# Kernel tuning notes

Hardware: AMD Instinct MI355X
Metric: run time of the kernel (lower is better)

## Reference

```python
import jax, jax.numpy as jnp
import numpy as np
import math

HIDDEN = 2048
N_Q = 16
N_KV = 8
HEAD_DIM = 128
THETA = 10000.0
RANK = 8
ALPHA = 16
LORA_SCALING = ALPHA / RANK  # 2.0
SCALING = 1.0 / math.sqrt(HEAD_DIM)


def setup_inputs() -> dict:
    key = jax.random.key(0)
    ks = jax.random.split(key, 14)
    B, S = 2, 2048
    std = 0.02
    inp = {
        "x": jax.random.normal(ks[0], (B, S, HIDDEN), dtype=jnp.float32),
        # nn.Linear weights: [out_features, in_features]
        "Wq": jax.random.normal(ks[1], (N_Q * HEAD_DIM, HIDDEN), dtype=jnp.float32) * std,
        "Wk": jax.random.normal(ks[2], (N_KV * HEAD_DIM, HIDDEN), dtype=jnp.float32) * std,
        "Wv": jax.random.normal(ks[3], (N_KV * HEAD_DIM, HIDDEN), dtype=jnp.float32) * std,
        "Wo": jax.random.normal(ks[4], (HIDDEN, N_Q * HEAD_DIM), dtype=jnp.float32) * std,
        "qA": jax.random.normal(ks[5], (RANK, HIDDEN), dtype=jnp.float32) * std,
        "qB": jax.random.normal(ks[6], (N_Q * HEAD_DIM, RANK), dtype=jnp.float32) * std,
        "kA": jax.random.normal(ks[7], (RANK, HIDDEN), dtype=jnp.float32) * std,
        "kB": jax.random.normal(ks[8], (N_KV * HEAD_DIM, RANK), dtype=jnp.float32) * std,
        "vA": jax.random.normal(ks[9], (RANK, HIDDEN), dtype=jnp.float32) * std,
        "vB": jax.random.normal(ks[10], (N_KV * HEAD_DIM, RANK), dtype=jnp.float32) * std,
        "oA": jax.random.normal(ks[11], (RANK, N_Q * HEAD_DIM), dtype=jnp.float32) * std,
        "oB": jax.random.normal(ks[12], (HIDDEN, RANK), dtype=jnp.float32) * std,
    }
    return inp


def _rope_cos_sin(seq_len, dtype):
    inv_freq = 1.0 / (THETA ** (jnp.arange(0, HEAD_DIM, 2, dtype=jnp.float32) / HEAD_DIM))
    t = jnp.arange(seq_len, dtype=jnp.float32)
    freqs = t[:, None] * inv_freq[None, :]  # [S, D/2]
    return jnp.cos(freqs).astype(dtype), jnp.sin(freqs).astype(dtype)


def _apply_rope(x, cos, sin):
    # x: [B, H, S, D]; interleaved real/imag pairs on last dim
    xr = x[..., ::2]
    xi = x[..., 1::2]
    rr = xr * cos - xi * sin
    ri = xr * sin + xi * cos
    return jnp.stack([rr, ri], axis=-1).reshape(x.shape)


def _forward(x, Wq, Wk, Wv, Wo, qA, qB, kA, kB, vA, vB, oA, oB):
    B, S, H = x.shape
    # base projections + LoRA (low-rank path kept factored: (x @ A^T) @ B^T)
    q = x @ Wq.T + ((x @ qA.T) @ qB.T) * LORA_SCALING  # [B,S,NQ*D]
    k = x @ Wk.T + ((x @ kA.T) @ kB.T) * LORA_SCALING  # [B,S,NKV*D]
    v = x @ Wv.T + ((x @ vA.T) @ vB.T) * LORA_SCALING
    q = q.reshape(B, S, N_Q, HEAD_DIM).transpose(0, 2, 1, 3)   # [B,NQ,S,D]
    k = k.reshape(B, S, N_KV, HEAD_DIM).transpose(0, 2, 1, 3)  # [B,NKV,S,D]
    v = v.reshape(B, S, N_KV, HEAD_DIM).transpose(0, 2, 1, 3)
    cos, sin = _rope_cos_sin(S, x.dtype)  # [S, D/2] each
    q = _apply_rope(q, cos, sin)
    k = _apply_rope(k, cos, sin)
    if N_Q != N_KV:
        rep = N_Q // N_KV
        k = jnp.repeat(k, rep, axis=1)  # [B,NQ,S,D]
        v = jnp.repeat(v, rep, axis=1)
    scores = jnp.einsum('bhqd,bhkd->bhqk', q, k) * SCALING
    causal = jnp.tril(jnp.ones((S, S), dtype=bool))
    scores = jnp.where(causal, scores, -jnp.inf)
    attn = jax.nn.softmax(scores, axis=-1).astype(v.dtype)
    out = jnp.einsum('bhqk,bhkd->bhqd', attn, v)  # [B,NQ,S,D]
    out = out.transpose(0, 2, 1, 3).reshape(B, S, N_Q * HEAD_DIM)
    return out @ Wo.T + ((out @ oA.T) @ oB.T) * LORA_SCALING


def reference(x, Wq, Wk, Wv, Wo, qA, qB, kA, kB, vA, vB, oA, oB):
    return _forward(x, Wq, Wk, Wv, Wo, qA, qB, kA, kB, vA, vB, oA, oB)
```

## Files before the change

### kernel.cpp

```cpp
#include <hip/hip_runtime.h>
#include <hip/hip_bf16.h>
#include <cmath>

#define HIDDEN 2048
#define SEQ 2048
#define BATCH 2
#define NQ 16
#define NKV 8
#define HD 128
#define RANKL 8
#define LORA_SCALE 2.0f
#define INV_SQRT_D 0.08838834764831845f
#define LOG2E 1.4426950408889634f
#define SM_SCALE (INV_SQRT_D * LOG2E)

typedef unsigned short ushort_t;
typedef __bf16 bf16x8 __attribute__((ext_vector_type(8)));
typedef float f32x4 __attribute__((ext_vector_type(4)));

static __device__ __forceinline__ ushort_t f2bf(float f) {
    __hip_bfloat16 h = __float2bfloat16(f);
    return *(ushort_t*)&h;
}
static __device__ __forceinline__ float bf2f(ushort_t u) {
    unsigned int v = ((unsigned int)u) << 16;
    return __builtin_bit_cast(float, v);
}
static __device__ __forceinline__ void gload_lds16(const ushort_t* g, ushort_t* l) {
    __builtin_amdgcn_global_load_lds(
        (const __attribute__((address_space(1))) unsigned int*)g,
        (__attribute__((address_space(3))) unsigned int*)l, 16, 0, 0);
}

__global__ __launch_bounds__(256) void lora_cast_x(
    const float* __restrict__ X, ushort_t* __restrict__ Xbf,
    const float* __restrict__ qA, const float* __restrict__ kA,
    const float* __restrict__ vA,
    float* __restrict__ oq, float* __restrict__ ok, float* __restrict__ ov)
{
    int m = blockIdx.x;
    int t = threadIdx.x;
    int c0 = t * 8;
    const float* xr = X + (size_t)m * HIDDEN + c0;
    float4 a = *(const float4*)xr;
    float4 b = *(const float4*)(xr + 4);
    float xv[8] = {a.x, a.y, a.z, a.w, b.x, b.y, b.z, b.w};
    uint4 o;
    o.x = (unsigned int)f2bf(xv[0]) | ((unsigned int)f2bf(xv[1]) << 16);
    o.y = (unsigned int)f2bf(xv[2]) | ((unsigned int)f2bf(xv[3]) << 16);
    o.z = (unsigned int)f2bf(xv[4]) | ((unsigned int)f2bf(xv[5]) << 16);
    o.w = (unsigned int)f2bf(xv[6]) | ((unsigned int)f2bf(xv[7]) << 16);
    *(uint4*)(Xbf + (size_t)m * HIDDEN + c0) = o;

    float p[3][RANKL];
#pragma unroll
    for (int w = 0; w < 3; w++)
#pragma unroll
        for (int r = 0; r < RANKL; r++) p[w][r] = 0.f;
    const float* Aw[3] = {qA, kA, vA};
#pragma unroll
    for (int e = 0; e < 8; e++) {
        float x8 = xv[e];
#pragma unroll
        for (int w = 0; w < 3; w++)
#pragma unroll
            for (int r = 0; r < RANKL; r++)
                p[w][r] += x8 * Aw[w][r * HIDDEN + c0 + e];
    }
#pragma unroll
    for (int w = 0; w < 3; w++)
#pragma unroll
        for (int r = 0; r < RANKL; r++) {
            float v = p[w][r];
            v += __shfl_xor(v, 32); v += __shfl_xor(v, 16);
            v += __shfl_xor(v, 8);  v += __shfl_xor(v, 4);
            v += __shfl_xor(v, 2);  v += __shfl_xor(v, 1);
            p[w][r] = v;
        }
    __shared__ float wred[4][3][RANKL];
    int wave = t >> 6, lane = t & 63;
    if (lane == 0) {
#pragma unroll
        for (int w = 0; w < 3; w++)
#pragma unroll
            for (int r = 0; r < RANKL; r++) wred[wave][w][r] = p[w][r];
    }
    __syncthreads();
    if (t < 3 * RANKL) {
        int w = t / RANKL, r = t % RANKL;
        float s = wred[0][w][r] + wred[1][w][r] + wred[2][w][r] + wred[3][w][r];
        float* dst = (w == 0) ? oq : (w == 1) ? ok : ov;
        dst[(size_t)m * RANKL + r] = s;
    }
}

__global__ __launch_bounds__(256) void lora_xa_bf16(
    const ushort_t* __restrict__ X, const float* __restrict__ Aw,
    float* __restrict__ out, int K)
{
    int m = blockIdx.x;
    int t = threadIdx.x;
    const ushort_t* xr = X + (size_t)m * K;
    float p[RANKL];
#pragma unroll
    for (int r = 0; r < RANKL; r++) p[r] = 0.f;
    for (int c = t; c < K; c += 256) {
        float xv = bf2f(xr[c]);
#pragma unroll
        for (int r = 0; r < RANKL; r++) p[r] += xv * Aw[r * K + c];
    }
#pragma unroll
    for (int r = 0; r < RANKL; r++) {
        float v = p[r];
        v += __shfl_xor(v, 32); v += __shfl_xor(v, 16);
        v += __shfl_xor(v, 8);  v += __shfl_xor(v, 4);
        v += __shfl_xor(v, 2);  v += __shfl_xor(v, 1);
        p[r] = v;
    }
    __shared__ float wred[4][RANKL];
    int wave = t >> 6, lane = t & 63;
    if (lane == 0) {
#pragma unroll
        for (int r = 0; r < RANKL; r++) wred[wave][r] = p[r];
    }
    __syncthreads();
    if (t < RANKL) {
        out[(size_t)m * RANKL + t] =
            wred[0][t] + wred[1][t] + wred[2][t] + wred[3][t];
    }
}

__global__ __launch_bounds__(256) void cast_weights(
    const float* __restrict__ Wq, const float* __restrict__ Wk,
    const float* __restrict__ Wv, const float* __restrict__ Wo,
    ushort_t* __restrict__ Wqb, ushort_t* __restrict__ Wkb,
    ushort_t* __restrict__ Wvb, ushort_t* __restrict__ Wob)
{
    size_t i = (size_t)blockIdx.x * 256 + threadIdx.x;
    const float* src; ushort_t* dst; size_t j;
    if (i < 524288)       { src = Wq; dst = Wqb; j = i; }
    else if (i < 786432)  { src = Wk; dst = Wkb; j = i - 524288; }
    else if (i < 1048576) { src = Wv; dst = Wvb; j = i - 786432; }
    else                  { src = Wo; dst = Wob; j = i - 1048576; }
    const float4* p = (const float4*)src + j * 2;
    float4 a = p[0], b = p[1];
    uint4 o;
    o.x = (unsigned int)f2bf(a.x) | ((unsigned int)f2bf(a.y) << 16);
    o.y = (unsigned int)f2bf(a.z) | ((unsigned int)f2bf(a.w) << 16);
    o.z = (unsigned int)f2bf(b.x) | ((unsigned int)f2bf(b.y) << 16);
    o.w = (unsigned int)f2bf(b.z) | ((unsigned int)f2bf(b.w) << 16);
    *(uint4*)(dst + j * 8) = o;
}

static __device__ __forceinline__ void gemm_core(
    const ushort_t* __restrict__ A, const ushort_t* __restrict__ B,
    void* __restrict__ Cout, int N, int K, int bm, int bn,
    const float* __restrict__ xa, const float* __restrict__ LB,
    float lscale, int out_bf16, ushort_t* As, ushort_t* Bs)
{
    const int t = threadIdx.x;
    const int lane = t & 63;
    const int w = t >> 6;
    const int quad = lane >> 4;
    const int c = lane & 15;

    const int wm = (w & 1) * 64;
    const int wn = (w >> 1) * 64;

    f32x4 acc[4][4];
#pragma unroll
    for (int i = 0; i < 4; i++)
#pragma unroll
        for (int j = 0; j < 4; j++) acc[i][j] = (f32x4){0.f, 0.f, 0.f, 0.f};

    const int p0 = w * 64 + lane;
    const int p1 = 256 + w * 64 + lane;
    const int r0 = p0 >> 2, g0 = (p0 & 3) ^ ((p0 >> 3) & 3);
    const int r1 = p1 >> 2, g1 = (p1 & 3) ^ ((p1 >> 3) & 3);
    const ushort_t* gA0 = A + (size_t)(bm + r0) * K + g0 * 8;
    const ushort_t* gA1 = A + (size_t)(bm + r1) * K + g1 * 8;
    const ushort_t* gB0 = B + (size_t)(bn + r0) * K + g0 * 8;
    const ushort_t* gB1 = B + (size_t)(bn + r1) * K + g1 * 8;
    ushort_t* lA0 = As + (size_t)(w * 64) * 8;
    ushort_t* lA1 = As + (size_t)(256 + w * 64) * 8;
    ushort_t* lB0 = Bs + (size_t)(w * 64) * 8;
    ushort_t* lB1 = Bs + (size_t)(256 + w * 64) * 8;

    const int csw = quad ^ ((c >> 1) & 3);

    for (int k0 = 0; k0 < K; k0 += 32) {
        __syncthreads();
        gload_lds16(gA0 + k0, lA0);
        gload_lds16(gA1 + k0, lA1);
        gload_lds16(gB0 + k0, lB0);
        gload_lds16(gB1 + k0, lB1);
        __syncthreads();

        bf16x8 af[4], bfr[4];
#pragma unroll
        for (int mt = 0; mt < 4; mt++)
            af[mt] = *(const bf16x8*)&As[((wm + mt * 16 + c) * 4 + csw) * 8];
#pragma unroll
        for (int nt = 0; nt < 4; nt++)
            bfr[nt] = *(const bf16x8*)&Bs[((wn + nt * 16 + c) * 4 + csw) * 8];
#pragma unroll
        for (int mt = 0; mt < 4; mt++)
#pragma unroll
            for (int nt = 0; nt < 4; nt++)
                acc[mt][nt] = __builtin_amdgcn_mfma_f32_16x16x32_bf16(
                    af[mt], bfr[nt], acc[mt][nt], 0, 0, 0);
    }

    float lb[4][RANKL];
#pragma unroll
    for (int nt = 0; nt < 4; nt++) {
        int col = bn + wn + nt * 16 + c;
        float4 u = *(const float4*)&LB[(size_t)col * RANKL];
        float4 v = *(const float4*)&LB[(size_t)col * RANKL + 4];
        lb[nt][0] = u.x; lb[nt][1] = u.y; lb[nt][2] = u.z; lb[nt][3] = u.w;
        lb[nt][4] = v.x; lb[nt][5] = v.y; lb[nt][6] = v.z; lb[nt][7] = v.w;
    }
#pragma unroll
    for (int mt = 0; mt < 4; mt++) {
        float la[4][RANKL];
#pragma unroll
        for (int r = 0; r < 4; r++) {
            int row = bm + wm + mt * 16 + quad * 4 + r;
            float4 u = *(const float4*)&xa[(size_t)row * RANKL];
            float4 v = *(const float4*)&xa[(size_t)row * RANKL + 4];
            la[r][0] = u.x; la[r][1] = u.y; la[r][2] = u.z; la[r][3] = u.w;
            la[r][4] = v.x; la[r][5] = v.y; la[r][6] = v.z; la[r][7] = v.w;
        }
#pragma unroll
        for (int nt = 0; nt < 4; nt++) {
#pragma unroll
            for (int r = 0; r < 4; r++) {
                float s = 0.f;
#pragma unroll
                for (int k = 0; k < RANKL; k++) s += la[r][k] * lb[nt][k];
                float val = acc[mt][nt][r] + lscale * s;
                size_t row = bm + wm + mt * 16 + quad * 4 + r;
                size_t col = bn + wn + nt * 16 + c;
                if (out_bf16)
                    ((ushort_t*)Cout)[row * N + col] = f2bf(val);
                else
                    ((float*)Cout)[row * N + col] = val;
            }
        }
    }
}

__global__ __launch_bounds__(256) void gemm_qkv(
    const ushort_t* __restrict__ A,
    const ushort_t* __restrict__ Wqb, const ushort_t* __restrict__ Wkb,
    const ushort_t* __restrict__ Wvb,
    ushort_t* __restrict__ q_lin, ushort_t* __restrict__ k_lin,
    ushort_t* __restrict__ v_lin,
    const float* __restrict__ xa_q, const float* __restrict__ xa_k,
    const float* __restrict__ xa_v,
    const float* __restrict__ qB, const float* __restrict__ kB,
    const float* __restrict__ vB)
{
    __shared__ ushort_t As[128 * 32];
    __shared__ ushort_t Bs[128 * 32];
    int bc = blockIdx.y;
    const ushort_t* B; ushort_t* Cout; const float* xa; const float* LB;
    int N, bn;
    if (bc < 16)      { B = Wqb; Cout = q_lin; xa = xa_q; LB = qB; N = 2048; bn = bc * 128; }
    else if (bc < 24) { B = Wkb; Cout = k_lin; xa = xa_k; LB = kB; N = 1024; bn = (bc - 16) * 128; }
    else              { B = Wvb; Cout = v_lin; xa = xa_v; LB = vB; N = 1024; bn = (bc - 24) * 128; }
    gemm_core(A, B, Cout, N, HIDDEN, blockIdx.x * 128, bn, xa, LB,
              LORA_SCALE, 1, As, Bs);
}

__global__ __launch_bounds__(256) void gemm_wo(
    const ushort_t* __restrict__ A, const ushort_t* __restrict__ Wob,
    float* __restrict__ out, const float* __restrict__ xa_o,
    const float* __restrict__ oB)
{
    __shared__ ushort_t As[128 * 32];
    __shared__ ushort_t Bs[128 * 32];
    gemm_core(A, Wob, out, HIDDEN, NQ * HD, blockIdx.x * 128, blockIdx.y * 128,
              xa_o, oB, LORA_SCALE, 0, As, Bs);
}

__global__ __launch_bounds__(256) void rope_qk(
    const ushort_t* __restrict__ qlin, const ushort_t* __restrict__ klin,
    ushort_t* __restrict__ qb, ushort_t* __restrict__ kb)
{
    int bs = blockIdx.x;
    int s = bs & (SEQ - 1);
    int b = bs >> 11;
    int t = threadIdx.x;
    int p = t & 63;
    float inv = exp2f(-(float)p * 0.20762050593046f);
    float ang = (float)s * inv;
    float cc = cosf(ang), si = sinf(ang);
#pragma unroll
    for (int j = 0; j < 6; j++) {
        int item = t + 256 * j;
        int hh = item >> 6;
        unsigned int pk;
        ushort_t* dst;
        if (hh < NQ) {
            pk = *(const unsigned int*)&qlin[(size_t)bs * (NQ * HD) + hh * HD + 2 * p];
            dst = qb + (((size_t)(b * NQ + hh) * SEQ) + s) * HD + 2 * p;
        } else {
            int kh = hh - NQ;
            pk = *(const unsigned int*)&klin[(size_t)bs * (NKV * HD) + kh * HD + 2 * p];
            dst = kb + (((size_t)(b * NKV + kh) * SEQ) + s) * HD + 2 * p;
        }
        float xr = bf2f((ushort_t)(pk & 0xffff));
        float xi = bf2f((ushort_t)(pk >> 16));
        float rr = xr * cc - xi * si;
        float ri = xr * si + xi * cc;
        *(unsigned int*)dst = ((unsigned int)f2bf(ri) << 16) | f2bf(rr);
    }
}

__global__ __launch_bounds__(256) void v_transpose(
    const ushort_t* __restrict__ vlin, ushort_t* __restrict__ Vt)
{
    int bk = blockIdx.x;
    int b = bk >> 3, kvh = bk & 7;
    int s0 = blockIdx.y * 64, d0 = blockIdx.z * 64;
    __shared__ ushort_t tile[64 * 72];
    int t = threadIdx.x;
#pragma unroll
    for (int i = 0; i < 2; i++) {
        int id = t + 256 * i;
        int r = id >> 3, cc = id & 7;
        uint4 v = *(const uint4*)&vlin[(size_t)(b * SEQ + s0 + r) * (NKV * HD)
                                       + kvh * HD + d0 + cc * 8];
        *(uint4*)&tile[r * 72 + cc * 8] = v;
    }
    __syncthreads();
#pragma unroll
    for (int i = 0; i < 2; i++) {
        int id = t + 256 * i;
        int dr = id >> 3, sc = id & 7;
        ushort_t tmp[8];
#pragma unroll
        for (int e = 0; e < 8; e++) tmp[e] = tile[(sc * 8 + e) * 72 + dr];
        *(uint4*)&Vt[((size_t)(b * NKV + kvh) * HD + d0 + dr) * SEQ + s0 + sc * 8]
            = *(uint4*)tmp;
    }
}

__global__ __launch_bounds__(256, 2) void attn_mfma3(
    const ushort_t* __restrict__ Q, const ushort_t* __restrict__ K,
    const ushort_t* __restrict__ V, ushort_t* __restrict__ O)
{
    __shared__ ushort_t Ks[2][64 * 128];
    __shared__ ushort_t Vs[2][128 * 64];
    __shared__ ushort_t Psh[4][16 * 68];

    const int t = threadIdx.x;
    const int lane = t & 63;
    const int w = t >> 6;
    const int quad = lane >> 4;
    const int c = lane & 15;
    const int q4 = quad * 4;
    const int c7 = c & 7;

    const int head = blockIdx.x >> 4;
    const int a = blockIdx.x & 15;
    const int h = head & (NQ - 1);
    const int b = head >> 4;
    const int kvh = b * NKV + (h >> 1);

    const ushort_t* Kg = K + (size_t)kvh * SEQ * HD;
    const ushort_t* Vg = V + (size_t)kvh * HD * SEQ;

    const ushort_t* gK[4]; const ushort_t* gV[4];
    int lo[4];
#pragma unroll
    for (int i = 0; i < 4; i++) {
        int cid = t + 256 * i;
        int kr = cid >> 4, kc = cid & 15;
        gK[i] = Kg + (size_t)kr * HD + ((kc ^ (kr & 7)) * 8);
        int vd = cid >> 3, vc = cid & 7;
        gV[i] = Vg + (size_t)vd * SEQ + ((vc ^ (vd & 7)) * 8);
        lo[i] = (i * 256 + (t & ~63)) * 8;
    }

#pragma unroll 1
    for (int half = 0; half < 2; half++) {
        const int qt = half ? (31 - a) : a;
        const int qb0 = qt * 64;
        const int myrow = qb0 + w * 16;

        const ushort_t* Qg = Q + ((size_t)head * SEQ + myrow + c) * HD;
        bf16x8 qf[4];
#pragma unroll
        for (int ch = 0; ch < 4; ch++)
            qf[ch] = *(const bf16x8*)(Qg + ch * 32 + quad * 8);

        f32x4 o[8];
#pragma unroll
        for (int i = 0; i < 8; i++) o[i] = (f32x4){0.f, 0.f, 0.f, 0.f};
        float lp[4] = {0.f, 0.f, 0.f, 0.f};

        const int ntiles = qt + 1;

#pragma unroll
        for (int i = 0; i < 4; i++) gload_lds16(gK[i], &Ks[0][lo[i]]);
#pragma unroll
        for (int i = 0; i < 4; i++) gload_lds16(gV[i], &Vs[0][lo[i]]);
        __syncthreads();

        for (int tile = 0; tile < ntiles; ++tile) {
            const int cur = tile & 1;
            if (tile + 1 < ntiles) {
                const int j1 = (tile + 1) * 64;
#pragma unroll
                for (int i = 0; i < 4; i++)
                    gload_lds16(gK[i] + (size_t)j1 * HD, &Ks[cur ^ 1][lo[i]]);
#pragma unroll
                for (int i = 0; i < 4; i++)
                    gload_lds16(gV[i] + j1, &Vs[cur ^ 1][lo[i]]);
            }

            f32x4 s[4];
#pragma unroll
            for (int tt = 0; tt < 4; tt++) s[tt] = (f32x4){0.f, 0.f, 0.f, 0.f};
#pragma unroll
            for (int tt = 0; tt < 4; tt++) {
                const int krow = tt * 16 + c;
#pragma unroll
                for (int ch = 0; ch < 4; ch++) {
                    bf16x8 kf = *(const bf16x8*)
                        &Ks[cur][krow * 128 + (((ch * 4 + quad) ^ c7) * 8)];
                    s[tt] = __builtin_amdgcn_mfma_f32_16x16x32_bf16(
                        qf[ch], kf, s[tt], 0, 0, 0);
                }
            }

            const bool diag = (tile == qt);
            const int j0 = tile * 64;
#pragma unroll
            for (int r = 0; r < 4; r++) {
                const int row_g = myrow + q4 + r;
#pragma unroll
                for (int tt = 0; tt < 4; tt++) {
                    float p = exp2f(s[tt][r] * SM_SCALE);
                    if (diag && (j0 + tt * 16 + c > row_g)) p = 0.f;
                    Psh[w][(q4 + r) * 68 + tt * 16 + c] = f2bf(p);
                    lp[r] += p;
                }
            }

            bf16x8 pf[2];
#pragma unroll
            for (int ch = 0; ch < 2; ch++) {
                int base = c * 68 + ch * 32 + quad * 8;
                uint2 aa = *(const uint2*)&Psh[w][base];
                uint2 bb = *(const uint2*)&Psh[w][base + 4];
                uint4 u; u.x = aa.x; u.y = aa.y; u.z = bb.x; u.w = bb.y;
                pf[ch] = __builtin_bit_cast(bf16x8, u);
            }

#pragma unroll
            for (int dt = 0; dt < 8; dt++) {
                const int vrow = dt * 16 + c;
#pragma unroll
                for (int ch = 0; ch < 2; ch++) {
                    bf16x8 vf = *(const bf16x8*)
                        &Vs[cur][vrow * 64 + (((ch * 4 + quad) ^ c7) * 8)];
                    o[dt] = __builtin_amdgcn_mfma_f32_16x16x32_bf16(
                        pf[ch], vf, o[dt], 0, 0, 0);
                }
            }
            __syncthreads();
        }

        float inv[4];
#pragma unroll
        for (int r = 0; r < 4; r++) {
            float v = lp[r];
            v += __shfl_xor(v, 1);
            v += __shfl_xor(v, 2);
            v += __shfl_xor(v, 4);
            v += __shfl_xor(v, 8);
            inv[r] = 1.f / v;
        }
        size_t base = ((size_t)b * SEQ + myrow + q4) * (NQ * HD) + h * HD + c;
#pragma unroll
        for (int r = 0; r < 4; r++)
#pragma unroll
            for (int dt = 0; dt < 8; dt++)
                O[base + (size_t)r * (NQ * HD) + dt * 16] =
                    f2bf(o[dt][r] * inv[r]);
    }
}

extern "C" void kernel_launch(void* const* d_in, const int* in_sizes, int n_in,
                              void* d_out, int out_size, void* d_ws, size_t ws_size,
                              hipStream_t stream)
{
    const float* x  = (const float*)d_in[0];
    const float* Wq = (const float*)d_in[1];
    const float* Wk = (const float*)d_in[2];
    const float* Wv = (const float*)d_in[3];
    const float* Wo = (const float*)d_in[4];
    const float* qA = (const float*)d_in[5];
    const float* qB = (const float*)d_in[6];
    const float* kA = (const float*)d_in[7];
    const float* kB = (const float*)d_in[8];
    const float* vA = (const float*)d_in[9];
    const float* vB = (const float*)d_in[10];
    const float* oA = (const float*)d_in[11];
    const float* oB = (const float*)d_in[12];
    float* out = (float*)d_out;
    float* ws = (float*)d_ws;

    const int M = BATCH * SEQ;

    float* xa_q = ws;
    float* xa_k = ws + 32768;
    float* xa_v = ws + 65536;
    float* xa_o = ws + 98304;
    ushort_t* q_lin = (ushort_t*)(ws + 131072);
    ushort_t* k_lin = (ushort_t*)(ws + 4325376);
    ushort_t* v_lin = (ushort_t*)(ws + 6422528);
    ushort_t* qb    = (ushort_t*)(ws + 8519680);
    ushort_t* kb    = (ushort_t*)(ws + 12713984);
    ushort_t* vtb   = (ushort_t*)(ws + 14811136);
    ushort_t* xbf   = (ushort_t*)(ws + 16908288);
    ushort_t* Wqb   = (ushort_t*)(ws + 21102592);
    ushort_t* Wkb   = (ushort_t*)(ws + 23199744);
    ushort_t* Wvb   = (ushort_t*)(ws + 24248320);
    ushort_t* Wob   = (ushort_t*)(ws + 25296896);
    ushort_t* attn_out = q_lin;

    lora_cast_x<<<M, 256, 0, stream>>>(x, xbf, qA, kA, vA, xa_q, xa_k, xa_v);

    cast_weights<<<6144, 256, 0, stream>>>(Wq, Wk, Wv, Wo, Wqb, Wkb, Wvb, Wob);

    gemm_qkv<<<dim3(M / 128, 32), 256, 0, stream>>>(
        xbf, Wqb, Wkb, Wvb, q_lin, k_lin, v_lin,
        xa_q, xa_k, xa_v, qB, kB, vB);

    rope_qk<<<M, 256, 0, stream>>>(q_lin, k_lin, qb, kb);
    v_transpose<<<dim3(BATCH * NKV, SEQ / 64, HD / 64), 256, 0, stream>>>(v_lin, vtb);

    attn_mfma3<<<512, 256, 0, stream>>>(qb, kb, vtb, attn_out);

    lora_xa_bf16<<<M, 256, 0, stream>>>(attn_out, oA, xa_o, NQ * HD);
    gemm_wo<<<dim3(M / 128, HIDDEN / 128), 256, 0, stream>>>(
        attn_out, Wob, out, xa_o, oB);
}
```

Baseline: 419.9 us.

## Fuse RoPE and V transpose into QKV GEMM epilogue, merge prep kernels

Merges the x cast/LoRA-A, weight cast and a new RoPE cos/sin table build into one prep launch. The QKV GEMM epilogue now applies RoPE directly, using a lane shuffle to fetch the pair partner, and writes Q and K in head-major layout and V transposed. This removes the separate rope and transpose kernels and their intermediate round-trip through global memory. The attention kernel drops K/V double buffering for a single buffer and raises the occupancy hint to 3, giving up load/compute overlap in exchange for more resident blocks. The epilogue stores become scattered 2-byte writes, which may coalesce poorly.

```diff
diff --git a/kernel.cpp b/kernel.cpp
--- a/kernel.cpp
+++ b/kernel.cpp
@@ -32,14 +32,48 @@
         (__attribute__((address_space(3))) unsigned int*)l, 16, 0, 0);
 }
 
-__global__ __launch_bounds__(256) void lora_cast_x(
+__global__ __launch_bounds__(256) void prep_kernel(
     const float* __restrict__ X, ushort_t* __restrict__ Xbf,
     const float* __restrict__ qA, const float* __restrict__ kA,
     const float* __restrict__ vA,
-    float* __restrict__ oq, float* __restrict__ ok, float* __restrict__ ov)
+    float* __restrict__ oq, float* __restrict__ ok, float* __restrict__ ov,
+    const float* __restrict__ Wq, const float* __restrict__ Wk,
+    const float* __restrict__ Wv, const float* __restrict__ Wo,
+    ushort_t* __restrict__ Wqb, ushort_t* __restrict__ Wkb,
+    ushort_t* __restrict__ Wvb, ushort_t* __restrict__ Wob,
+    float2* __restrict__ rope_tab)
 {
-    int m = blockIdx.x;
-    int t = threadIdx.x;
+    __shared__ float wred[4][3][RANKL];
+    const int blk = blockIdx.x;
+    const int t = threadIdx.x;
+
+    if (blk >= 10240) {
+        int idx = (blk - 10240) * 256 + t;
+        int s = idx >> 6, p = idx & 63;
+        float inv = exp2f(-(float)p * 0.20762050593046f);
+        float ang = (float)s * inv;
+        rope_tab[idx] = make_float2(cosf(ang), sinf(ang));
+        return;
+    }
+    if (blk >= 4096) {
+        size_t i = (size_t)(blk - 4096) * 256 + t;
+        const float* src; ushort_t* dst; size_t j;
+        if (i < 524288)       { src = Wq; dst = Wqb; j = i; }
+        else if (i < 786432)  { src = Wk; dst = Wkb; j = i - 524288; }
+        else if (i < 1048576) { src = Wv; dst = Wvb; j = i - 786432; }
+        else                  { src = Wo; dst = Wob; j = i - 1048576; }
+        const float4* p = (const float4*)src + j * 2;
+        float4 a = p[0], b = p[1];
+        uint4 o;
+        o.x = (unsigned int)f2bf(a.x) | ((unsigned int)f2bf(a.y) << 16);
+        o.y = (unsigned int)f2bf(a.z) | ((unsigned int)f2bf(a.w) << 16);
+        o.z = (unsigned int)f2bf(b.x) | ((unsigned int)f2bf(b.y) << 16);
+        o.w = (unsigned int)f2bf(b.z) | ((unsigned int)f2bf(b.w) << 16);
+        *(uint4*)(dst + j * 8) = o;
+        return;
+    }
+
+    int m = blk;
     int c0 = t * 8;
     const float* xr = X + (size_t)m * HIDDEN + c0;
     float4 a = *(const float4*)xr;
@@ -77,7 +111,6 @@
             v += __shfl_xor(v, 2);  v += __shfl_xor(v, 1);
             p[w][r] = v;
         }
-    __shared__ float wred[4][3][RANKL];
     int wave = t >> 6, lane = t & 63;
     if (lane == 0) {
 #pragma unroll
@@ -130,42 +163,39 @@
     }
 }
 
-__global__ __launch_bounds__(256) void cast_weights(
-    const float* __restrict__ Wq, const float* __restrict__ Wk,
-    const float* __restrict__ Wv, const float* __restrict__ Wo,
-    ushort_t* __restrict__ Wqb, ushort_t* __restrict__ Wkb,
-    ushort_t* __restrict__ Wvb, ushort_t* __restrict__ Wob)
+__global__ __launch_bounds__(256) void gemm_qkv(
+    const ushort_t* __restrict__ A,
+    const ushort_t* __restrict__ Wqb, const ushort_t* __restrict__ Wkb,
+    const ushort_t* __restrict__ Wvb,
+    ushort_t* __restrict__ qb, ushort_t* __restrict__ kb,
+    ushort_t* __restrict__ vtb,
+    const float* __restrict__ xa_q, const float* __restrict__ xa_k,
+    const float* __restrict__ xa_v,
+    const float* __restrict__ qB, const float* __restrict__ kB,
+    const float* __restrict__ vB,
+    const float2* __restrict__ rope_tab)
 {
-    size_t i = (size_t)blockIdx.x * 256 + threadIdx.x;
-    const float* src; ushort_t* dst; size_t j;
-    if (i < 524288)       { src = Wq; dst = Wqb; j = i; }
-    else if (i < 786432)  { src = Wk; dst = Wkb; j = i - 524288; }
-    else if (i < 1048576) { src = Wv; dst = Wvb; j = i - 786432; }
-    else                  { src = Wo; dst = Wob; j = i - 1048576; }
-    const float4* p = (const float4*)src + j * 2;
-    float4 a = p[0], b = p[1];
-    uint4 o;
-    o.x = (unsigned int)f2bf(a.x) | ((unsigned int)f2bf(a.y) << 16);
-    o.y = (unsigned int)f2bf(a.z) | ((unsigned int)f2bf(a.w) << 16);
-    o.z = (unsigned int)f2bf(b.x) | ((unsigned int)f2bf(b.y) << 16);
-    o.w = (unsigned int)f2bf(b.z) | ((unsigned int)f2bf(b.w) << 16);
-    *(uint4*)(dst + j * 8) = o;
-}
-
-static __device__ __forceinline__ void gemm_core(
-    const ushort_t* __restrict__ A, const ushort_t* __restrict__ B,
-    void* __restrict__ Cout, int N, int K, int bm, int bn,
-    const float* __restrict__ xa, const float* __restrict__ LB,
-    float lscale, int out_bf16, ushort_t* As, ushort_t* Bs)
-{
+    __shared__ ushort_t As[128 * 32];
+    __shared__ ushort_t Bs[128 * 32];
+
     const int t = threadIdx.x;
     const int lane = t & 63;
     const int w = t >> 6;
     const int quad = lane >> 4;
     const int c = lane & 15;
+    const int q4 = quad * 4;
+
+    const int bm = blockIdx.x * 128;
+    const int bc = blockIdx.y;
+    int mode, bn;
+    const ushort_t* B; const float* xa; const float* LB;
+    if (bc < 16)      { mode = 0; B = Wqb; xa = xa_q; LB = qB; bn = bc * 128; }
+    else if (bc < 24) { mode = 1; B = Wkb; xa = xa_k; LB = kB; bn = (bc - 16) * 128; }
+    else              { mode = 2; B = Wvb; xa = xa_v; LB = vB; bn = (bc - 24) * 128; }
 
     const int wm = (w & 1) * 64;
     const int wn = (w >> 1) * 64;
+    const int K = HIDDEN;
 
     f32x4 acc[4][4];
 #pragma unroll
@@ -211,6 +241,7 @@
                     af[mt], bfr[nt], acc[mt][nt], 0, 0, 0);
     }
 
+    const int b = bm >> 11;
     float lb[4][RANKL];
 #pragma unroll
     for (int nt = 0; nt < 4; nt++) {
@@ -220,57 +251,59 @@
         lb[nt][0] = u.x; lb[nt][1] = u.y; lb[nt][2] = u.z; lb[nt][3] = u.w;
         lb[nt][4] = v.x; lb[nt][5] = v.y; lb[nt][6] = v.z; lb[nt][7] = v.w;
     }
+    const float ssign = (c & 1) ? 1.f : -1.f;
+
 #pragma unroll
     for (int mt = 0; mt < 4; mt++) {
         float la[4][RANKL];
 #pragma unroll
         for (int r = 0; r < 4; r++) {
-            int row = bm + wm + mt * 16 + quad * 4 + r;
+            int row = bm + wm + mt * 16 + q4 + r;
             float4 u = *(const float4*)&xa[(size_t)row * RANKL];
             float4 v = *(const float4*)&xa[(size_t)row * RANKL + 4];
             la[r][0] = u.x; la[r][1] = u.y; la[r][2] = u.z; la[r][3] = u.w;
             la[r][4] = v.x; la[r][5] = v.y; la[r][6] = v.z; la[r][7] = v.w;
         }
+        const int s0 = (bm + wm + mt * 16 + q4) & (SEQ - 1);
 #pragma unroll
         for (int nt = 0; nt < 4; nt++) {
+            const int col = bn + wn + nt * 16 + c;
+            const int d = col & (HD - 1);
+            float vals[4];
 #pragma unroll
             for (int r = 0; r < 4; r++) {
                 float s = 0.f;
 #pragma unroll
                 for (int k = 0; k < RANKL; k++) s += la[r][k] * lb[nt][k];
-                float val = acc[mt][nt][r] + lscale * s;
-                size_t row = bm + wm + mt * 16 + quad * 4 + r;
-                size_t col = bn + wn + nt * 16 + c;
-                if (out_bf16)
-                    ((ushort_t*)Cout)[row * N + col] = f2bf(val);
-                else
-                    ((float*)Cout)[row * N + col] = val;
-            }
-        }
-    }
-}
-
-__global__ __launch_bounds__(256) void gemm_qkv(
-    const ushort_t* __restrict__ A,
-    const ushort_t* __restrict__ Wqb, const ushort_t* __restrict__ Wkb,
-    const ushort_t* __restrict__ Wvb,
-    ushort_t* __restrict__ q_lin, ushort_t* __restrict__ k_lin,
-    ushort_t* __restrict__ v_lin,
-    const float* __restrict__ xa_q, const float* __restrict__ xa_k,
-    const float* __restrict__ xa_v,
-    const float* __restrict__ qB, const float* __restrict__ kB,
-    const float* __restrict__ vB)
-{
-    __shared__ ushort_t As[128 * 32];
-    __shared__ ushort_t Bs[128 * 32];
-    int bc = blockIdx.y;
-    const ushort_t* B; ushort_t* Cout; const float* xa; const float* LB;
-    int N, bn;
-    if (bc < 16)      { B = Wqb; Cout = q_lin; xa = xa_q; LB = qB; N = 2048; bn = bc * 128; }
-    else if (bc < 24) { B = Wkb; Cout = k_lin; xa = xa_k; LB = kB; N = 1024; bn = (bc - 16) * 128; }
-    else              { B = Wvb; Cout = v_lin; xa = xa_v; LB = vB; N = 1024; bn = (bc - 24) * 128; }
-    gemm_core(A, B, Cout, N, HIDDEN, blockIdx.x * 128, bn, xa, LB,
-              LORA_SCALE, 1, As, Bs);
+                vals[r] = acc[mt][nt][r] + LORA_SCALE * s;
+            }
+            if (mode == 2) {
+                const int kvh = col >> 7;
+                ushort_t pack[4];
+#pragma unroll
+                for (int r = 0; r < 4; r++) pack[r] = f2bf(vals[r]);
+                *(uint2*)&vtb[((size_t)(b * NKV + kvh) * HD + d) * SEQ + s0]
+                    = *(uint2*)pack;
+            } else {
+                const int pq = d >> 1;
+#pragma unroll
+                for (int r = 0; r < 4; r++) {
+                    float pv = __shfl_xor(vals[r], 1);
+                    float2 cs = rope_tab[(size_t)(s0 + r) * 64 + pq];
+                    float out = vals[r] * cs.x + pv * ssign * cs.y;
+                    if (mode == 0) {
+                        const int hh = col >> 7;
+                        qb[((size_t)(b * NQ + hh) * SEQ + s0 + r) * HD + d]
+                            = f2bf(out);
+                    } else {
+                        const int kvh = col >> 7;
+                        kb[((size_t)(b * NKV + kvh) * SEQ + s0 + r) * HD + d]
+                            = f2bf(out);
+                    }
+                }
+            }
+        }
+    }
 }
 
 __global__ __launch_bounds__(256) void gemm_wo(
@@ -280,79 +313,105 @@
 {
     __shared__ ushort_t As[128 * 32];
     __shared__ ushort_t Bs[128 * 32];
-    gemm_core(A, Wob, out, HIDDEN, NQ * HD, blockIdx.x * 128, blockIdx.y * 128,
-              xa_o, oB, LORA_SCALE, 0, As, Bs);
-}
-
-__global__ __launch_bounds__(256) void rope_qk(
-    const ushort_t* __restrict__ qlin, const ushort_t* __restrict__ klin,
-    ushort_t* __restrict__ qb, ushort_t* __restrict__ kb)
-{
-    int bs = blockIdx.x;
-    int s = bs & (SEQ - 1);
-    int b = bs >> 11;
-    int t = threadIdx.x;
-    int p = t & 63;
-    float inv = exp2f(-(float)p * 0.20762050593046f);
-    float ang = (float)s * inv;
-    float cc = cosf(ang), si = sinf(ang);
-#pragma unroll
-    for (int j = 0; j < 6; j++) {
-        int item = t + 256 * j;
-        int hh = item >> 6;
-        unsigned int pk;
-        ushort_t* dst;
-        if (hh < NQ) {
-            pk = *(const unsigned int*)&qlin[(size_t)bs * (NQ * HD) + hh * HD + 2 * p];
-            dst = qb + (((size_t)(b * NQ + hh) * SEQ) + s) * HD + 2 * p;
-        } else {
-            int kh = hh - NQ;
-            pk = *(const unsigned int*)&klin[(size_t)bs * (NKV * HD) + kh * HD + 2 * p];
-            dst = kb + (((size_t)(b * NKV + kh) * SEQ) + s) * HD + 2 * p;
-        }
-        float xr = bf2f((ushort_t)(pk & 0xffff));
-        float xi = bf2f((ushort_t)(pk >> 16));
-        float rr = xr * cc - xi * si;
-        float ri = xr * si + xi * cc;
-        *(unsigned int*)dst = ((unsigned int)f2bf(ri) << 16) | f2bf(rr);
-    }
-}
-
-__global__ __launch_bounds__(256) void v_transpose(
-    const ushort_t* __restrict__ vlin, ushort_t* __restrict__ Vt)
-{
-    int bk = blockIdx.x;
-    int b = bk >> 3, kvh = bk & 7;
-    int s0 = blockIdx.y * 64, d0 = blockIdx.z * 64;
-    __shared__ ushort_t tile[64 * 72];
-    int t = threadIdx.x;
-#pragma unroll
-    for (int i = 0; i < 2; i++) {
-        int id = t + 256 * i;
-        int r = id >> 3, cc = id & 7;
-        uint4 v = *(const uint4*)&vlin[(size_t)(b * SEQ + s0 + r) * (NKV * HD)
-                                       + kvh * HD + d0 + cc * 8];
-        *(uint4*)&tile[r * 72 + cc * 8] = v;
-    }
-    __syncthreads();
-#pragma unroll
-    for (int i = 0; i < 2; i++) {
-        int id = t + 256 * i;
-        int dr = id >> 3, sc = id & 7;
-        ushort_t tmp[8];
-#pragma unroll
-        for (int e = 0; e < 8; e++) tmp[e] = tile[(sc * 8 + e) * 72 + dr];
-        *(uint4*)&Vt[((size_t)(b * NKV + kvh) * HD + d0 + dr) * SEQ + s0 + sc * 8]
-            = *(uint4*)tmp;
-    }
-}
-
-__global__ __launch_bounds__(256, 2) void attn_mfma3(
+
+    const int t = threadIdx.x;
+    const int lane = t & 63;
+    const int w = t >> 6;
+    const int quad = lane >> 4;
+    const int c = lane & 15;
+
+    const int bm = blockIdx.x * 128;
+    const int bn = blockIdx.y * 128;
+    const int wm = (w & 1) * 64;
+    const int wn = (w >> 1) * 64;
+    const int K = NQ * HD;
+    const int N = HIDDEN;
+
+    f32x4 acc[4][4];
+#pragma unroll
+    for (int i = 0; i < 4; i++)
+#pragma unroll
+        for (int j = 0; j < 4; j++) acc[i][j] = (f32x4){0.f, 0.f, 0.f, 0.f};
+
+    const int p0 = w * 64 + lane;
+    const int p1 = 256 + w * 64 + lane;
+    const int r0 = p0 >> 2, g0 = (p0 & 3) ^ ((p0 >> 3) & 3);
+    const int r1 = p1 >> 2, g1 = (p1 & 3) ^ ((p1 >> 3) & 3);
+    const ushort_t* gA0 = A + (size_t)(bm + r0) * K + g0 * 8;
+    const ushort_t* gA1 = A + (size_t)(bm + r1) * K + g1 * 8;
+    const ushort_t* gB0 = Wob + (size_t)(bn + r0) * K + g0 * 8;
+    const ushort_t* gB1 = Wob + (size_t)(bn + r1) * K + g1 * 8;
+    ushort_t* lA0 = As + (size_t)(w * 64) * 8;
+    ushort_t* lA1 = As + (size_t)(256 + w * 64) * 8;
+    ushort_t* lB0 = Bs + (size_t)(w * 64) * 8;
+    ushort_t* lB1 = Bs + (size_t)(256 + w * 64) * 8;
+
+    const int csw = quad ^ ((c >> 1) & 3);
+
+    for (int k0 = 0; k0 < K; k0 += 32) {
+        __syncthreads();
+        gload_lds16(gA0 + k0, lA0);
+        gload_lds16(gA1 + k0, lA1);
+        gload_lds16(gB0 + k0, lB0);
+        gload_lds16(gB1 + k0, lB1);
+        __syncthreads();
+
+        bf16x8 af[4], bfr[4];
+#pragma unroll
+        for (int mt = 0; mt < 4; mt++)
+            af[mt] = *(const bf16x8*)&As[((wm + mt * 16 + c) * 4 + csw) * 8];
+#pragma unroll
+        for (int nt = 0; nt < 4; nt++)
+            bfr[nt] = *(const bf16x8*)&Bs[((wn + nt * 16 + c) * 4 + csw) * 8];
+#pragma unroll
+        for (int mt = 0; mt < 4; mt++)
+#pragma unroll
+            for (int nt = 0; nt < 4; nt++)
+                acc[mt][nt] = __builtin_amdgcn_mfma_f32_16x16x32_bf16(
+                    af[mt], bfr[nt], acc[mt][nt], 0, 0, 0);
+    }
+
+    float lb[4][RANKL];
+#pragma unroll
+    for (int nt = 0; nt < 4; nt++) {
+        int col = bn + wn + nt * 16 + c;
+        float4 u = *(const float4*)&oB[(size_t)col * RANKL];
+        float4 v = *(const float4*)&oB[(size_t)col * RANKL + 4];
+        lb[nt][0] = u.x; lb[nt][1] = u.y; lb[nt][2] = u.z; lb[nt][3] = u.w;
+        lb[nt][4] = v.x; lb[nt][5] = v.y; lb[nt][6] = v.z; lb[nt][7] = v.w;
+    }
+#pragma unroll
+    for (int mt = 0; mt < 4; mt++) {
+        float la[4][RANKL];
+#pragma unroll
+        for (int r = 0; r < 4; r++) {
+            int row = bm + wm + mt * 16 + (lane >> 4) * 4 + r;
+            float4 u = *(const float4*)&xa_o[(size_t)row * RANKL];
+            float4 v = *(const float4*)&xa_o[(size_t)row * RANKL + 4];
+            la[r][0] = u.x; la[r][1] = u.y; la[r][2] = u.z; la[r][3] = u.w;
+            la[r][4] = v.x; la[r][5] = v.y; la[r][6] = v.z; la[r][7] = v.w;
+        }
+#pragma unroll
+        for (int nt = 0; nt < 4; nt++) {
+#pragma unroll
+            for (int r = 0; r < 4; r++) {
+                float s = 0.f;
+#pragma unroll
+                for (int k = 0; k < RANKL; k++) s += la[r][k] * lb[nt][k];
+                size_t row = bm + wm + mt * 16 + quad * 4 + r;
+                size_t col = bn + wn + nt * 16 + c;
+                out[row * N + col] = acc[mt][nt][r] + LORA_SCALE * s;
+            }
+        }
+    }
+}
+
+__global__ __launch_bounds__(256, 3) void attn_mfma4(
     const ushort_t* __restrict__ Q, const ushort_t* __restrict__ K,
     const ushort_t* __restrict__ V, ushort_t* __restrict__ O)
 {
-    __shared__ ushort_t Ks[2][64 * 128];
-    __shared__ ushort_t Vs[2][128 * 64];
+    __shared__ ushort_t Ks[64 * 128];
+    __shared__ ushort_t Vs[128 * 64];
     __shared__ ushort_t Psh[4][16 * 68];
 
     const int t = threadIdx.x;
@@ -403,23 +462,16 @@
 
         const int ntiles = qt + 1;
 
-#pragma unroll
-        for (int i = 0; i < 4; i++) gload_lds16(gK[i], &Ks[0][lo[i]]);
-#pragma unroll
-        for (int i = 0; i < 4; i++) gload_lds16(gV[i], &Vs[0][lo[i]]);
-        __syncthreads();
-
         for (int tile = 0; tile < ntiles; ++tile) {
-            const int cur = tile & 1;
-            if (tile + 1 < ntiles) {
-                const int j1 = (tile + 1) * 64;
-#pragma unroll
-                for (int i = 0; i < 4; i++)
-                    gload_lds16(gK[i] + (size_t)j1 * HD, &Ks[cur ^ 1][lo[i]]);
-#pragma unroll
-                for (int i = 0; i < 4; i++)
-                    gload_lds16(gV[i] + j1, &Vs[cur ^ 1][lo[i]]);
-            }
+            const int j0 = tile * 64;
+            __syncthreads();
+#pragma unroll
+            for (int i = 0; i < 4; i++)
+                gload_lds16(gK[i] + (size_t)j0 * HD, &Ks[lo[i]]);
+#pragma unroll
+            for (int i = 0; i < 4; i++)
+                gload_lds16(gV[i] + j0, &Vs[lo[i]]);
+            __syncthreads();
 
             f32x4 s[4];
 #pragma unroll
@@ -430,14 +482,13 @@
 #pragma unroll
                 for (int ch = 0; ch < 4; ch++) {
                     bf16x8 kf = *(const bf16x8*)
-                        &Ks[cur][krow * 128 + (((ch * 4 + quad) ^ c7) * 8)];
+                        &Ks[krow * 128 + (((ch * 4 + quad) ^ c7) * 8)];
                     s[tt] = __builtin_amdgcn_mfma_f32_16x16x32_bf16(
                         qf[ch], kf, s[tt], 0, 0, 0);
                 }
             }
 
             const bool diag = (tile == qt);
-            const int j0 = tile * 64;
 #pragma unroll
             for (int r = 0; r < 4; r++) {
                 const int row_g = myrow + q4 + r;
@@ -466,12 +517,11 @@
 #pragma unroll
                 for (int ch = 0; ch < 2; ch++) {
                     bf16x8 vf = *(const bf16x8*)
-                        &Vs[cur][vrow * 64 + (((ch * 4 + quad) ^ c7) * 8)];
+                        &Vs[vrow * 64 + (((ch * 4 + quad) ^ c7) * 8)];
                     o[dt] = __builtin_amdgcn_mfma_f32_16x16x32_bf16(
                         pf[ch], vf, o[dt], 0, 0, 0);
                 }
             }
-            __syncthreads();
         }
 
         float inv[4];
@@ -520,31 +570,26 @@
     float* xa_k = ws + 32768;
     float* xa_v = ws + 65536;
     float* xa_o = ws + 98304;
-    ushort_t* q_lin = (ushort_t*)(ws + 131072);
-    ushort_t* k_lin = (ushort_t*)(ws + 4325376);
-    ushort_t* v_lin = (ushort_t*)(ws + 6422528);
-    ushort_t* qb    = (ushort_t*)(ws + 8519680);
-    ushort_t* kb    = (ushort_t*)(ws + 12713984);
-    ushort_t* vtb   = (ushort_t*)(ws + 14811136);
-    ushort_t* xbf   = (ushort_t*)(ws + 16908288);
-    ushort_t* Wqb   = (ushort_t*)(ws + 21102592);
-    ushort_t* Wkb   = (ushort_t*)(ws + 23199744);
-    ushort_t* Wvb   = (ushort_t*)(ws + 24248320);
-    ushort_t* Wob   = (ushort_t*)(ws + 25296896);
-    ushort_t* attn_out = q_lin;
-
-    lora_cast_x<<<M, 256, 0, stream>>>(x, xbf, qA, kA, vA, xa_q, xa_k, xa_v);
-
-    cast_weights<<<6144, 256, 0, stream>>>(Wq, Wk, Wv, Wo, Wqb, Wkb, Wvb, Wob);
+    float2* rope_tab = (float2*)(ws + 131072);
+    ushort_t* qb  = (ushort_t*)(ws + 393216);
+    ushort_t* kb  = (ushort_t*)(ws + 4587520);
+    ushort_t* vtb = (ushort_t*)(ws + 6684672);
+    ushort_t* attn_out = (ushort_t*)(ws + 8781824);
+    ushort_t* xbf = (ushort_t*)(ws + 12976128);
+    ushort_t* Wqb = (ushort_t*)(ws + 17170432);
+    ushort_t* Wkb = (ushort_t*)(ws + 19267584);
+    ushort_t* Wvb = (ushort_t*)(ws + 20316160);
+    ushort_t* Wob = (ushort_t*)(ws + 21364736);
+
+    prep_kernel<<<10752, 256, 0, stream>>>(
+        x, xbf, qA, kA, vA, xa_q, xa_k, xa_v,
+        Wq, Wk, Wv, Wo, Wqb, Wkb, Wvb, Wob, rope_tab);
 
     gemm_qkv<<<dim3(M / 128, 32), 256, 0, stream>>>(
-        xbf, Wqb, Wkb, Wvb, q_lin, k_lin, v_lin,
-        xa_q, xa_k, xa_v, qB, kB, vB);
-
-    rope_qk<<<M, 256, 0, stream>>>(q_lin, k_lin, qb, kb);
-    v_transpose<<<dim3(BATCH * NKV, SEQ / 64, HD / 64), 256, 0, stream>>>(v_lin, vtb);
-
-    attn_mfma3<<<512, 256, 0, stream>>>(qb, kb, vtb, attn_out);
+        xbf, Wqb, Wkb, Wvb, qb, kb, vtb,
+        xa_q, xa_k, xa_v, qB, kB, vB, rope_tab);
+
+    attn_mfma4<<<512, 256, 0, stream>>>(qb, kb, vtb, attn_out);
 
     lora_xa_bf16<<<M, 256, 0, stream>>>(attn_out, oA, xa_o, NQ * HD);
     gemm_wo<<<dim3(M / 128, HIDDEN / 128), 256, 0, stream>>>(
```

After: 426.0 us. No clear change (+1.5%).
